# Optimization experiments

Measured on AMD Instinct MI355X. Metric: run time of the kernel, lower is better.

## Reference

```python
import jax, jax.numpy as jnp
import numpy as np
from jax import lax

SLOPE = 0.01  # nn.LeakyReLU default negative slope

def leaky(x):
    return jnp.where(x >= 0, x, SLOPE * x)

def conv2d(x, w, b, pad):
    # x: [N,C,H,W], w: [O,I,kh,kw]
    y = lax.conv_general_dilated(x, w, (1, 1), [(pad, pad), (pad, pad)],
                                 dimension_numbers=('NCHW', 'OIHW', 'NCHW'))
    return y + b[None, :, None, None]

def centered_ifftn(x, axes):
    # np.fft.fftshift(np.fft.ifftn(np.fft.ifftshift(X), norm='ortho'))
    return jnp.fft.fftshift(jnp.fft.ifftn(jnp.fft.ifftshift(x, axes=axes), axes=axes, norm='ortho'), axes=axes)

def setup_inputs() -> dict:
    key = jax.random.key(0)
    ks = jax.random.split(key, 10)
    B, H, W, CK = 8, 640, 368, 32
    return {
        'img':    jax.random.normal(ks[0], (B, 1, H, W), jnp.float32),
        'kspace': jax.random.normal(ks[1], (B, 2, H, W), jnp.float32),
        # k_model1: Conv2d(2, CK, 3, padding=1) + LeakyReLU
        'wk': jax.random.normal(ks[2], (CK, 2, 3, 3), jnp.float32) * 0.1,
        'bk': jnp.zeros((CK,), jnp.float32),
        # conv1: Conv2d(CK, 2, kernel_size=1)
        'w1': jax.random.normal(ks[3], (2, CK, 1, 1), jnp.float32) * 0.1,
        'b1': jnp.zeros((2,), jnp.float32),
        # conv2: Conv2d(2, 1, kernel_size=1)
        'w2': jax.random.normal(ks[4], (1, 2, 1, 1), jnp.float32) * 0.1,
        'b2': jnp.zeros((1,), jnp.float32),
        # i_model1: Conv2d(1, 1, 3, padding=1) + LeakyReLU
        'wi': jax.random.normal(ks[5], (1, 1, 3, 3), jnp.float32) * 0.1,
        'bi': jnp.zeros((1,), jnp.float32),
    }

def reference(img, kspace, wk, bk, w1, b1, w2, b2, wi, bi):
    # k-space branch: k_model1 then conv1 + LeakyReLU
    out1 = leaky(conv2d(leaky(conv2d(kspace, wk, bk, 1)), w1, b1, 0))  # [B,2,H,W]
    # channel 0 = real, channel 1 = imag; ifftn over ALL axes (incl. batch),
    # exactly as the original numpy call with axes=range(out.ndim)
    cplx = out1[:, 0].astype(jnp.complex64) + 1j * out1[:, 1].astype(jnp.complex64)  # [B,H,W]
    im = jnp.abs(centered_ifftn(cplx, (0, 1, 2)))[:, None]  # [B,1,H,W]
    # concat with image, cast to half (torch.cuda.HalfTensor), conv2 + LeakyReLU
    out = jnp.concatenate([im, img], axis=1).astype(jnp.float16)  # [B,2,H,W]
    out = leaky(conv2d(out, w2.astype(jnp.float16), b2.astype(jnp.float16), 0))
    out = out.astype(jnp.float32)  # [B,1,H,W]
    # image-domain model
    return leaky(conv2d(out, wi, bi, 1))  # [B,1,H,W]
```

## Files before the change

### kernel.cpp

```cpp
#include <hip/hip_runtime.h>
#include <hip/hip_fp16.h>
#include <math.h>

#define B_ 8
#define H_ 640
#define W_ 368
#define HW_ (H_*W_)
#define NP_ (B_*H_*W_)

#define FROWS 4
#define HLINES 4
#define HP 645
#define TS 16

typedef __attribute__((ext_vector_type(8))) short v8s;
typedef __attribute__((ext_vector_type(4))) float v4f;

__device__ __forceinline__ float leaky_(float x){ return fmaxf(x, 0.01f*x); }

__device__ __forceinline__ unsigned short f2bf(float x){
    unsigned u = __float_as_uint(x);
    u += 0x7FFFu + ((u >> 16) & 1u);
    return (unsigned short)(u >> 16);
}

__device__ __forceinline__ float2 cadd_(float2 a, float2 b){ return make_float2(a.x+b.x, a.y+b.y); }
__device__ __forceinline__ float2 csub_(float2 a, float2 b){ return make_float2(a.x-b.x, a.y-b.y); }
__device__ __forceinline__ float2 cmul_(float2 a, float c, float s){
    return make_float2(a.x*c - a.y*s, a.x*s + a.y*c);
}
__device__ __forceinline__ float2 cmulv_(float2 a, float2 w){
    return make_float2(a.x*w.x - a.y*w.y, a.x*w.y + a.y*w.x);
}

__device__ __forceinline__ void dft4p_(float2 p0, float2 p1, float2 p2, float2 p3,
                                       float2& z0, float2& z1, float2& z2, float2& z3){
    float2 s0 = cadd_(p0,p2), d0 = csub_(p0,p2);
    float2 s1 = cadd_(p1,p3), d1 = csub_(p1,p3);
    z0 = cadd_(s0,s1);
    z2 = csub_(s0,s1);
    z1 = make_float2(d0.x - d1.y, d0.y + d1.x);
    z3 = make_float2(d0.x + d1.y, d0.y - d1.x);
}

__device__ __forceinline__ void fft16p_(const float2* x, float2* X){
    const float C1 = 0.9238795325112867f, S1 = 0.3826834323650898f;
    const float R  = 0.7071067811865476f;
    float2 Y[4][4];
    #pragma unroll
    for (int b = 0; b < 4; ++b)
        dft4p_(x[b], x[4+b], x[8+b], x[12+b], Y[b][0], Y[b][1], Y[b][2], Y[b][3]);
    Y[1][1] = cmul_(Y[1][1],  C1,  S1);
    Y[1][2] = cmul_(Y[1][2],   R,   R);
    Y[1][3] = cmul_(Y[1][3],  S1,  C1);
    Y[2][1] = cmul_(Y[2][1],   R,   R);
    Y[2][2] = make_float2(-Y[2][2].y, Y[2][2].x);
    Y[2][3] = cmul_(Y[2][3],  -R,   R);
    Y[3][1] = cmul_(Y[3][1],  S1,  C1);
    Y[3][2] = cmul_(Y[3][2],  -R,   R);
    Y[3][3] = cmul_(Y[3][3], -C1, -S1);
    #pragma unroll
    for (int c = 0; c < 4; ++c)
        dft4p_(Y[0][c], Y[1][c], Y[2][c], Y[3][c], X[c], X[c+4], X[c+8], X[c+12]);
}

__device__ __forceinline__ void fft8p_(const float2* x, float2* X){
    const float R = 0.7071067811865476f;
    float2 Y0[4], Y1[4];
    dft4p_(x[0], x[2], x[4], x[6], Y0[0], Y0[1], Y0[2], Y0[3]);
    dft4p_(x[1], x[3], x[5], x[7], Y1[0], Y1[1], Y1[2], Y1[3]);
    float2 T0 = Y1[0];
    float2 T1 = cmul_(Y1[1],  R, R);
    float2 T2 = make_float2(-Y1[2].y, Y1[2].x);
    float2 T3 = cmul_(Y1[3], -R, R);
    X[0] = cadd_(Y0[0], T0);  X[4] = csub_(Y0[0], T0);
    X[1] = cadd_(Y0[1], T1);  X[5] = csub_(Y0[1], T1);
    X[2] = cadd_(Y0[2], T2);  X[6] = csub_(Y0[2], T2);
    X[3] = cadd_(Y0[3], T3);  X[7] = csub_(Y0[3], T3);
}

__global__ void init_tables_kernel(float2* __restrict__ T){
    int i = blockIdx.x*blockDim.x + threadIdx.x;
    if (i >= 1301) return;
    int r, c, modN; int j;
    if      (i <  368){ j = i;        r = j%16; c = j/16; modN = 368; }
    else if (i < 1008){ j = i-368;    r = j%16; c = j/16; modN = 640; }
    else if (i < 1048){ j = i-1008;   r = j%8;  c = j/8;  modN = 40;  }
    else              { j = i-1048;   r = j/11; c = j%11 + 1; modN = 23; }
    int t = (int)(((long long)r * c) % modN);
    if (t > modN/2) t -= modN;
    float ang = (float)(6.283185307179586 * ((double)t / (double)modN));
    float s, co;
    sincosf(ang, &s, &co);
    T[i] = make_float2(co, s);
}

__global__ __launch_bounds__(256) void kfftw_kernel(const float* __restrict__ ksp,
                               const float* __restrict__ wk,
                               const float* __restrict__ bk,
                               const float* __restrict__ w1,
                               const float* __restrict__ b1,
                               const float2* __restrict__ TW368P,
                               const float2* __restrict__ F23P,
                               float2* __restrict__ Bt){
    __shared__ unsigned short Sb[4836];
    __shared__ unsigned short Wr[4*512];
    __shared__ float2 X[FROWS*369];
    int t = threadIdx.x;
    int blk = blockIdx.x;
    int b  = blk / 160;
    int h0 = (blk - b*160) * FROWS;

    for (int seg = 0; seg < 12; ++seg){
        int r = seg >> 1, ic = seg & 1;
        int hh = h0 - 1 + r;
        int ok = ((unsigned)hh < 640u);
        const float* base = ksp + ((size_t)(b*2 + ic)*640 + (ok ? hh : 0))*368;
        for (int col = t; col < 372; col += 256){
            int c = col - 1;
            float v = (ok && (unsigned)c < 368u) ? base[c] : 0.f;
            Sb[seg*372 + col] = f2bf(v);
        }
    }
    for (int i = t; i < 372; i += 256) Sb[4464 + i] = 0;

    int lane = t & 63, wave = t >> 6;
    int oc = lane & 15, q = lane >> 4;
    int l = wave;

    int off[8];
    v8s bf0, bf1, b2f;
    #pragma unroll
    for (int j = 0; j < 8; ++j){
        int kk = q*8 + j;
        if (kk < 18){
            int ic = (kk >= 9) ? 1 : 0;
            int tt = kk - ic*9;
            int ty = tt/3, tx = tt - ty*3;
            off[j] = ((ty + l)*2 + ic)*372 + tx;
            bf0[j] = (short)f2bf(wk[oc*18 + kk]);
            bf1[j] = (short)f2bf(wk[(oc+16)*18 + kk]);
        } else {
            off[j] = 4464;
            bf0[j] = 0; bf1[j] = 0;
        }
        b2f[j] = (oc < 2) ? (short)f2bf(w1[oc*32 + kk]) : (short)0;
    }
    float bk0 = bk[oc], bk1 = bk[oc+16];
    float biasn = (oc == 1) ? b1[1] : b1[0];
    unsigned short* Wrw = Wr + (wave << 9);
    __syncthreads();

    for (int g = 0; g < 23; ++g){
        int w0m = g*16 + oc;
        v8s af;
        #pragma unroll
        for (int j = 0; j < 8; ++j) af[j] = (short)Sb[off[j] + w0m];
        v4f d0 = {0.f,0.f,0.f,0.f}, d1 = {0.f,0.f,0.f,0.f};
        d0 = __builtin_amdgcn_mfma_f32_16x16x32_bf16(af, bf0, d0, 0, 0, 0);
        d1 = __builtin_amdgcn_mfma_f32_16x16x32_bf16(af, bf1, d1, 0, 0, 0);
        #pragma unroll
        for (int r = 0; r < 4; ++r){
            int px = q*4 + r;
            Wrw[px*32 + oc]      = f2bf(leaky_(d0[r] + bk0));
            Wrw[px*32 + 16 + oc] = f2bf(leaky_(d1[r] + bk1));
        }
        asm volatile("s_waitcnt lgkmcnt(0)" ::: "memory");
        const v8s* ap = (const v8s*)(Wrw + oc*32);
        v8s a2 = ap[q];
        v4f d2 = {0.f,0.f,0.f,0.f};
        d2 = __builtin_amdgcn_mfma_f32_16x16x32_bf16(a2, b2f, d2, 0, 0, 0);
        float vals[4], ov[4];
        #pragma unroll
        for (int r = 0; r < 4; ++r){
            vals[r] = leaky_(biasn + d2[r]);
            ov[r] = __shfl_xor(vals[r], 1);
        }
        if (oc == 0){
            int px = g*16 + q*4;
            X[l*369 + px  ] = make_float2( vals[0],  ov[0]);
            X[l*369 + px+1] = make_float2(-vals[1], -ov[1]);
            X[l*369 + px+2] = make_float2( vals[2],  ov[2]);
            X[l*369 + px+3] = make_float2(-vals[3], -ov[3]);
        }
        asm volatile("s_waitcnt lgkmcnt(0)" ::: "memory");
    }
    __syncthreads();

    if (t < 92){
        int ll = t & 3, n2 = t >> 2;
        float2 xr[16], Xo[16];
        #pragma unroll
        for (int n1 = 0; n1 < 16; ++n1) xr[n1] = X[ll*369 + 23*n1 + n2];
        fft16p_(xr, Xo);
        const float2* row = TW368P + n2*16;
        #pragma unroll
        for (int k1 = 0; k1 < 16; ++k1)
            X[ll*369 + 23*k1 + n2] = cmulv_(Xo[k1], row[k1]);
    }
    __syncthreads();

    {
        int ll = t & 3, k1 = (t >> 2) & 15, qr = t >> 6;
        const float2* xp = X + ll*369 + 23*k1;
        float2 x0 = xp[0];
        float2 u[11], d[11];
        #pragma unroll
        for (int m = 1; m <= 11; ++m){
            float2 a = xp[m], bb = xp[23-m];
            u[m-1] = cadd_(a, bb);
            d[m-1] = csub_(a, bb);
        }
        __syncthreads();
        int k2beg = qr*6;
        int k2end = (qr == 3) ? 23 : k2beg + 6;
        for (int k2 = k2beg; k2 < k2end; ++k2){
            const float2* row = F23P + k2*11;
            float re = x0.x, im = x0.y;
            #pragma unroll
            for (int m = 0; m < 11; ++m){
                float c = row[m].x, s = row[m].y;
                re += u[m].x*c - d[m].y*s;
                im += u[m].y*c + d[m].x*s;
            }
            X[ll*369 + k1 + 16*k2] = make_float2(re, im);
        }
    }
    __syncthreads();

    const float sc = 0.052129458158616354f;
    for (int i = t; i < FROWS*368; i += 256){
        int k = i >> 2, ll = i & 3;
        float2 v = X[ll*369 + k];
        float s = (k & 1) ? -sc : sc;
        Bt[((size_t)(b*368 + k))*640 + h0 + ll] = make_float2(v.x*s, v.y*s);
    }
}

__global__ __launch_bounds__(256) void fftH_kernel(const float2* __restrict__ Bt,
                                                   const float2* __restrict__ TW640P,
                                                   const float2* __restrict__ TW40P,
                                                   float2* __restrict__ A2){
    __shared__ float2 X[HLINES*HP];
    int t = threadIdx.x;
    size_t base = (size_t)blockIdx.x * (HLINES*640);

    for (int i = t; i < HLINES*640; i += 256){
        int l = i / 640, n = i - l*640;
        float2 v = Bt[base + i];
        float s = (n & 1) ? -1.f : 1.f;
        X[l*HP + n] = make_float2(v.x*s, v.y*s);
    }
    __syncthreads();

    if (t < 160){
        int l = t & 3, n2 = t >> 2;
        float2 xr[16], Xo[16];
        #pragma unroll
        for (int n1 = 0; n1 < 16; ++n1) xr[n1] = X[l*HP + 40*n1 + n2];
        fft16p_(xr, Xo);
        const float2* row = TW640P + n2*16;
        #pragma unroll
        for (int k1 = 0; k1 < 16; ++k1)
            X[l*HP + 40*k1 + n2] = cmulv_(Xo[k1], row[k1]);
    }
    __syncthreads();

    for (int it = t; it < 320; it += 256){
        int l = it & 3, k1 = (it >> 2) & 15, m2 = it >> 6;
        float2 xr[8], Xo[8];
        #pragma unroll
        for (int m1 = 0; m1 < 8; ++m1) xr[m1] = X[l*HP + 40*k1 + 5*m1 + m2];
        fft8p_(xr, Xo);
        const float2* row = TW40P + m2*8;
        #pragma unroll
        for (int j1 = 0; j1 < 8; ++j1)
            X[l*HP + 40*k1 + 5*j1 + m2] = cmulv_(Xo[j1], row[j1]);
    }
    __syncthreads();

    {
        const float CK1[5] = {1.f,  0.30901699437494745f, -0.8090169943749475f, -0.8090169943749475f,  0.30901699437494745f};
        const float SK1[5] = {0.f,  0.9510565162951535f,   0.5877852522924731f, -0.5877852522924731f, -0.9510565162951535f};
        const float CK2[5] = {1.f, -0.8090169943749475f,   0.30901699437494745f, 0.30901699437494745f, -0.8090169943749475f};
        const float SK2[5] = {0.f,  0.5877852522924731f,  -0.9510565162951535f,  0.9510565162951535f, -0.5877852522924731f};
        int it0 = t, it1 = t + 256;
        int l0 = it0 & 3, k10 = (it0 >> 2) & 15, j10 = it0 >> 6;
        int l1 = it1 & 3, k11 = (it1 >> 2) & 15, j11 = it1 >> 6;
        float2 p0[5], p1[5];
        #pragma unroll
        for (int m2 = 0; m2 < 5; ++m2) p0[m2] = X[l0*HP + 40*k10 + 5*j10 + m2];
        #pragma unroll
        for (int m2 = 0; m2 < 5; ++m2) p1[m2] = X[l1*HP + 40*k11 + 5*j11 + m2];
        __syncthreads();
        float2 u0a = cadd_(p0[1], p0[4]), d0a = csub_(p0[1], p0[4]);
        float2 u0b = cadd_(p0[2], p0[3]), d0b = csub_(p0[2], p0[3]);
        float2 u1a = cadd_(p1[1], p1[4]), d1a = csub_(p1[1], p1[4]);
        float2 u1b = cadd_(p1[2], p1[3]), d1b = csub_(p1[2], p1[3]);
        #pragma unroll
        for (int j2 = 0; j2 < 5; ++j2){
            float c1v = CK1[j2], s1v = SK1[j2], c2v = CK2[j2], s2v = SK2[j2];
            float re0 = p0[0].x + u0a.x*c1v - d0a.y*s1v + u0b.x*c2v - d0b.y*s2v;
            float im0 = p0[0].y + u0a.y*c1v + d0a.x*s1v + u0b.y*c2v + d0b.x*s2v;
            float re1 = p1[0].x + u1a.x*c1v - d1a.y*s1v + u1b.x*c2v - d1b.y*s2v;
            float im1 = p1[0].y + u1a.y*c1v + d1a.x*s1v + u1b.y*c2v + d1b.x*s2v;
            X[l0*HP + k10 + 16*j10 + 128*j2] = make_float2(re0, im0);
            X[l1*HP + k11 + 16*j11 + 128*j2] = make_float2(re1, im1);
        }
    }
    __syncthreads();

    const float sc = 0.03952847075210474f;
    for (int i = t; i < HLINES*640; i += 256){
        int l = i / 640, k = i - l*640;
        float2 v = X[l*HP + k];
        float s = (k & 1) ? -sc : sc;
        A2[base + i] = make_float2(v.x*s, v.y*s);
    }
}

__global__ __launch_bounds__(256) void tail_kernel(const float2* __restrict__ A2,
                                  const float* __restrict__ img,
                                  const float* __restrict__ w2,
                                  const float* __restrict__ b2,
                                  const float* __restrict__ wi,
                                  const float* __restrict__ bi,
                                  float* __restrict__ out){
    __shared__ float Pl[8][TS+2][TS+3];
    int t = threadIdx.x;
    int ty0 = (blockIdx.x / 23) * TS;
    int tx0 = (blockIdx.x % 23) * TS;

    float w2h0 = __half2float(__float2half(w2[0]));
    float w2h1 = __half2float(__float2half(w2[1]));
    float b2h  = __half2float(__float2half(b2[0]));
    const float sc8 = 0.35355339059327373f;

    for (int idx = t; idx < (TS+2)*(TS+2); idx += 256){
        int hx = idx / (TS+2), hy = idx - hx*(TS+2);
        int hh = ty0 - 1 + hy, ww = tx0 - 1 + hx;
        int hc = min(max(hh, 0), H_-1), wc = min(max(ww, 0), W_-1);
        float2 x[8], Xo[8];
        #pragma unroll
        for (int n = 0; n < 8; ++n){
            float2 v = A2[((size_t)(n*368 + wc))*640 + hc];
            float s = (n & 1) ? -1.f : 1.f;
            x[n] = make_float2(v.x*s, v.y*s);
        }
        fft8p_(x, Xo);
        #pragma unroll
        for (int k = 0; k < 8; ++k){
            float s = (k & 1) ? -sc8 : sc8;
            float yr = Xo[k].x * s, yi = Xo[k].y * s;
            float mag = sqrtf(yr*yr + yi*yi);
            Pl[k][hy][hx] = __half2float(__float2half(mag));
        }
    }
    __syncthreads();

    for (int idx = t; idx < (TS+2)*(TS+2); idx += 256){
        int hy = idx / (TS+2), hx = idx - hy*(TS+2);
        int hh = ty0 - 1 + hy, ww = tx0 - 1 + hx;
        bool inb = (hh >= 0) && (hh < H_) && (ww >= 0) && (ww < W_);
        int hc = min(max(hh, 0), H_-1), wc = min(max(ww, 0), W_-1);
        float inbf = inb ? 1.f : 0.f;
        #pragma unroll
        for (int k = 0; k < 8; ++k){
            float g = __half2float(__float2half(img[(size_t)k*HW_ + hc*W_ + wc]));
            float a = Pl[k][hy][hx];
            float o = leaky_(a*w2h0 + g*w2h1 + b2h);
            o = __half2float(__float2half(o));
            Pl[k][hy][hx] = o * inbf;
        }
    }
    __syncthreads();

    int sy = t >> 4, sx = t & 15;
    float wv[9];
    #pragma unroll
    for (int q = 0; q < 9; ++q) wv[q] = wi[q];
    float bi0 = bi[0];
    #pragma unroll
    for (int k = 0; k < 8; ++k){
        float acc = bi0;
        #pragma unroll
        for (int dy = 0; dy < 3; ++dy)
            #pragma unroll
            for (int dx = 0; dx < 3; ++dx)
                acc += wv[dy*3+dx] * Pl[k][sy+dy][sx+dx];
        out[((size_t)k*H_ + ty0+sy)*W_ + tx0+sx] = leaky_(acc);
    }
}

extern "C" void kernel_launch(void* const* d_in, const int* in_sizes, int n_in,
                              void* d_out, int out_size, void* d_ws, size_t ws_size,
                              hipStream_t stream){
    const float* img = (const float*)d_in[0];
    const float* ksp = (const float*)d_in[1];
    const float* wk  = (const float*)d_in[2];
    const float* bk  = (const float*)d_in[3];
    const float* w1  = (const float*)d_in[4];
    const float* b1  = (const float*)d_in[5];
    const float* w2  = (const float*)d_in[6];
    const float* b2  = (const float*)d_in[7];
    const float* wi  = (const float*)d_in[8];
    const float* bi  = (const float*)d_in[9];

    char* ws = (char*)d_ws;
    float2* Bt  = (float2*)(ws + 0);
    float2* A2  = (float2*)(ws + 15073280);
    float2* T   = (float2*)(ws + 30146560);
    float2* TW368P = T + 0;
    float2* TW640P = T + 368;
    float2* TW40P  = T + 1008;
    float2* F23P   = T + 1048;
    float* out  = (float*)d_out;

    init_tables_kernel<<<6, 256, 0, stream>>>(T);

    kfftw_kernel<<<B_*(H_/FROWS), 256, 0, stream>>>(ksp, wk, bk, w1, b1,
                                                    TW368P, F23P, Bt);
    fftH_kernel<<<(B_*W_)/HLINES, 256, 0, stream>>>(Bt, TW640P, TW40P, A2);
    tail_kernel<<<(H_/TS)*(W_/TS), 256, 0, stream>>>(A2, img, w2, b2, wi, bi, out);
}
```

Baseline: 172.4 us.

## Fuse batch-axis FFT and magnitude into H-FFT kernel; widen k-space conv blocks

The H-axis FFT kernel now handles all 8 batch lines for one W column per block and finishes the length-8 batch-axis FFT plus the magnitude in shared memory. It writes a real float magnitude array instead of complex A2, so the tail kernel no longer redoes the batch FFT for every halo pixel and reads half as many bytes. The k-space conv/FFT kernel moves to 512 threads, with two waves splitting each row's column groups and the radix-23 stage spread over more threads. The trade-off is fewer blocks (368) in the H-FFT kernel, more work per block, and higher register pressure.

New measurement: 191.0 us. 1.11x slower.

```diff
diff --git a/kernel.cpp b/kernel.cpp
--- a/kernel.cpp
+++ b/kernel.cpp
@@ -9,7 +9,6 @@
 #define NP_ (B_*H_*W_)
 
 #define FROWS 4
-#define HLINES 4
 #define HP 645
 #define TS 16
 
@@ -95,7 +94,7 @@
     T[i] = make_float2(co, s);
 }
 
-__global__ __launch_bounds__(256) void kfftw_kernel(const float* __restrict__ ksp,
+__global__ __launch_bounds__(512) void kfftw_kernel(const float* __restrict__ ksp,
                                const float* __restrict__ wk,
                                const float* __restrict__ bk,
                                const float* __restrict__ w1,
@@ -104,7 +103,7 @@
                                const float2* __restrict__ F23P,
                                float2* __restrict__ Bt){
     __shared__ unsigned short Sb[4836];
-    __shared__ unsigned short Wr[4*512];
+    __shared__ unsigned short Wr[8*512];
     __shared__ float2 X[FROWS*369];
     int t = threadIdx.x;
     int blk = blockIdx.x;
@@ -116,17 +115,17 @@
         int hh = h0 - 1 + r;
         int ok = ((unsigned)hh < 640u);
         const float* base = ksp + ((size_t)(b*2 + ic)*640 + (ok ? hh : 0))*368;
-        for (int col = t; col < 372; col += 256){
+        for (int col = t; col < 372; col += 512){
             int c = col - 1;
             float v = (ok && (unsigned)c < 368u) ? base[c] : 0.f;
             Sb[seg*372 + col] = f2bf(v);
         }
     }
-    for (int i = t; i < 372; i += 256) Sb[4464 + i] = 0;
+    for (int i = t; i < 372; i += 512) Sb[4464 + i] = 0;
 
     int lane = t & 63, wave = t >> 6;
     int oc = lane & 15, q = lane >> 4;
-    int l = wave;
+    int l = wave >> 1, half = wave & 1;
 
     int off[8];
     v8s bf0, bf1, b2f;
@@ -151,7 +150,9 @@
     unsigned short* Wrw = Wr + (wave << 9);
     __syncthreads();
 
-    for (int g = 0; g < 23; ++g){
+    int gbeg = half ? 12 : 0;
+    int gend = half ? 23 : 12;
+    for (int g = gbeg; g < gend; ++g){
         int w0m = g*16 + oc;
         v8s af;
         #pragma unroll
@@ -201,7 +202,7 @@
     __syncthreads();
 
     {
-        int ll = t & 3, k1 = (t >> 2) & 15, qr = t >> 6;
+        int k1 = t & 15, ll = (t >> 4) & 3, eighth = t >> 6;
         const float2* xp = X + ll*369 + 23*k1;
         float2 x0 = xp[0];
         float2 u[11], d[11];
@@ -212,8 +213,8 @@
             d[m-1] = csub_(a, bb);
         }
         __syncthreads();
-        int k2beg = qr*6;
-        int k2end = (qr == 3) ? 23 : k2beg + 6;
+        int k2beg = eighth*3;
+        int k2end = min(k2beg + 3, 23);
         for (int k2 = k2beg; k2 < k2end; ++k2){
             const float2* row = F23P + k2*11;
             float re = x0.x, im = x0.y;
@@ -229,7 +230,7 @@
     __syncthreads();
 
     const float sc = 0.052129458158616354f;
-    for (int i = t; i < FROWS*368; i += 256){
+    for (int i = t; i < FROWS*368; i += 512){
         int k = i >> 2, ll = i & 3;
         float2 v = X[ll*369 + k];
         float s = (k & 1) ? -sc : sc;
@@ -237,24 +238,24 @@
     }
 }
 
-__global__ __launch_bounds__(256) void fftH_kernel(const float2* __restrict__ Bt,
-                                                   const float2* __restrict__ TW640P,
-                                                   const float2* __restrict__ TW40P,
-                                                   float2* __restrict__ A2){
-    __shared__ float2 X[HLINES*HP];
+__global__ __launch_bounds__(256) void ffthb_kernel(const float2* __restrict__ Bt,
+                                                    const float2* __restrict__ TW640P,
+                                                    const float2* __restrict__ TW40P,
+                                                    float* __restrict__ Mag){
+    __shared__ float2 X[8*HP];
     int t = threadIdx.x;
-    size_t base = (size_t)blockIdx.x * (HLINES*640);
-
-    for (int i = t; i < HLINES*640; i += 256){
+    int w = blockIdx.x;
+
+    for (int i = t; i < 8*640; i += 256){
         int l = i / 640, n = i - l*640;
-        float2 v = Bt[base + i];
+        float2 v = Bt[((size_t)(l*368 + w))*640 + n];
         float s = (n & 1) ? -1.f : 1.f;
         X[l*HP + n] = make_float2(v.x*s, v.y*s);
     }
     __syncthreads();
 
-    if (t < 160){
-        int l = t & 3, n2 = t >> 2;
+    for (int it = t; it < 320; it += 256){
+        int l = it & 7, n2 = it >> 3;
         float2 xr[16], Xo[16];
         #pragma unroll
         for (int n1 = 0; n1 < 16; ++n1) xr[n1] = X[l*HP + 40*n1 + n2];
@@ -266,8 +267,8 @@
     }
     __syncthreads();
 
-    for (int it = t; it < 320; it += 256){
-        int l = it & 3, k1 = (it >> 2) & 15, m2 = it >> 6;
+    for (int it = t; it < 640; it += 256){
+        int l = it & 7, k1 = (it >> 3) & 15, m2 = it >> 7;
         float2 xr[8], Xo[8];
         #pragma unroll
         for (int m1 = 0; m1 < 8; ++m1) xr[m1] = X[l*HP + 40*k1 + 5*m1 + m2];
@@ -284,42 +285,55 @@
         const float SK1[5] = {0.f,  0.9510565162951535f,   0.5877852522924731f, -0.5877852522924731f, -0.9510565162951535f};
         const float CK2[5] = {1.f, -0.8090169943749475f,   0.30901699437494745f, 0.30901699437494745f, -0.8090169943749475f};
         const float SK2[5] = {0.f,  0.5877852522924731f,  -0.9510565162951535f,  0.9510565162951535f, -0.5877852522924731f};
-        int it0 = t, it1 = t + 256;
-        int l0 = it0 & 3, k10 = (it0 >> 2) & 15, j10 = it0 >> 6;
-        int l1 = it1 & 3, k11 = (it1 >> 2) & 15, j11 = it1 >> 6;
-        float2 p0[5], p1[5];
-        #pragma unroll
-        for (int m2 = 0; m2 < 5; ++m2) p0[m2] = X[l0*HP + 40*k10 + 5*j10 + m2];
-        #pragma unroll
-        for (int m2 = 0; m2 < 5; ++m2) p1[m2] = X[l1*HP + 40*k11 + 5*j11 + m2];
+        float2 p[4][5];
+        int ui[4];
+        #pragma unroll
+        for (int i = 0; i < 4; ++i){
+            int u = t + 256*i;
+            ui[u >= 1024 ? 0 : i] = u;
+            ui[i] = u;
+            int l = u & 7, k1 = (u >> 3) & 15, j1 = u >> 7;
+            #pragma unroll
+            for (int m2 = 0; m2 < 5; ++m2)
+                p[i][m2] = X[l*HP + 40*k1 + 5*j1 + m2];
+        }
         __syncthreads();
-        float2 u0a = cadd_(p0[1], p0[4]), d0a = csub_(p0[1], p0[4]);
-        float2 u0b = cadd_(p0[2], p0[3]), d0b = csub_(p0[2], p0[3]);
-        float2 u1a = cadd_(p1[1], p1[4]), d1a = csub_(p1[1], p1[4]);
-        float2 u1b = cadd_(p1[2], p1[3]), d1b = csub_(p1[2], p1[3]);
-        #pragma unroll
-        for (int j2 = 0; j2 < 5; ++j2){
-            float c1v = CK1[j2], s1v = SK1[j2], c2v = CK2[j2], s2v = SK2[j2];
-            float re0 = p0[0].x + u0a.x*c1v - d0a.y*s1v + u0b.x*c2v - d0b.y*s2v;
-            float im0 = p0[0].y + u0a.y*c1v + d0a.x*s1v + u0b.y*c2v + d0b.x*s2v;
-            float re1 = p1[0].x + u1a.x*c1v - d1a.y*s1v + u1b.x*c2v - d1b.y*s2v;
-            float im1 = p1[0].y + u1a.y*c1v + d1a.x*s1v + u1b.y*c2v + d1b.x*s2v;
-            X[l0*HP + k10 + 16*j10 + 128*j2] = make_float2(re0, im0);
-            X[l1*HP + k11 + 16*j11 + 128*j2] = make_float2(re1, im1);
-        }
-    }
-    __syncthreads();
-
-    const float sc = 0.03952847075210474f;
-    for (int i = t; i < HLINES*640; i += 256){
-        int l = i / 640, k = i - l*640;
-        float2 v = X[l*HP + k];
-        float s = (k & 1) ? -sc : sc;
-        A2[base + i] = make_float2(v.x*s, v.y*s);
-    }
-}
-
-__global__ __launch_bounds__(256) void tail_kernel(const float2* __restrict__ A2,
+        #pragma unroll
+        for (int i = 0; i < 4; ++i){
+            int u = ui[i];
+            int l = u & 7, k1 = (u >> 3) & 15, j1 = u >> 7;
+            float2 ua = cadd_(p[i][1], p[i][4]), da = csub_(p[i][1], p[i][4]);
+            float2 ub = cadd_(p[i][2], p[i][3]), db = csub_(p[i][2], p[i][3]);
+            #pragma unroll
+            for (int j2 = 0; j2 < 5; ++j2){
+                float c1v = CK1[j2], s1v = SK1[j2], c2v = CK2[j2], s2v = SK2[j2];
+                float re = p[i][0].x + ua.x*c1v - da.y*s1v + ub.x*c2v - db.y*s2v;
+                float im = p[i][0].y + ua.y*c1v + da.x*s1v + ub.y*c2v + db.x*s2v;
+                X[l*HP + k1 + 16*j1 + 128*j2] = make_float2(re, im);
+            }
+        }
+    }
+    __syncthreads();
+
+    const float SC = 0.013975424859373685f;
+    for (int hh = t; hh < 640; hh += 256){
+        float2 x[8], Xo[8];
+        #pragma unroll
+        for (int l = 0; l < 8; ++l){
+            float2 v = X[l*HP + hh];
+            float s = (l & 1) ? -SC : SC;
+            x[l] = make_float2(v.x*s, v.y*s);
+        }
+        fft8p_(x, Xo);
+        #pragma unroll
+        for (int k = 0; k < 8; ++k){
+            float mag = sqrtf(Xo[k].x*Xo[k].x + Xo[k].y*Xo[k].y);
+            Mag[((size_t)(k*368 + w))*640 + hh] = mag;
+        }
+    }
+}
+
+__global__ __launch_bounds__(256) void tail_kernel(const float* __restrict__ Mag,
                                   const float* __restrict__ img,
                                   const float* __restrict__ w2,
                                   const float* __restrict__ b2,
@@ -334,25 +348,14 @@
     float w2h0 = __half2float(__float2half(w2[0]));
     float w2h1 = __half2float(__float2half(w2[1]));
     float b2h  = __half2float(__float2half(b2[0]));
-    const float sc8 = 0.35355339059327373f;
 
     for (int idx = t; idx < (TS+2)*(TS+2); idx += 256){
         int hx = idx / (TS+2), hy = idx - hx*(TS+2);
         int hh = ty0 - 1 + hy, ww = tx0 - 1 + hx;
         int hc = min(max(hh, 0), H_-1), wc = min(max(ww, 0), W_-1);
-        float2 x[8], Xo[8];
-        #pragma unroll
-        for (int n = 0; n < 8; ++n){
-            float2 v = A2[((size_t)(n*368 + wc))*640 + hc];
-            float s = (n & 1) ? -1.f : 1.f;
-            x[n] = make_float2(v.x*s, v.y*s);
-        }
-        fft8p_(x, Xo);
         #pragma unroll
         for (int k = 0; k < 8; ++k){
-            float s = (k & 1) ? -sc8 : sc8;
-            float yr = Xo[k].x * s, yi = Xo[k].y * s;
-            float mag = sqrtf(yr*yr + yi*yi);
+            float mag = Mag[((size_t)(k*368 + wc))*640 + hc];
             Pl[k][hy][hx] = __half2float(__float2half(mag));
         }
     }
@@ -408,7 +411,7 @@
 
     char* ws = (char*)d_ws;
     float2* Bt  = (float2*)(ws + 0);
-    float2* A2  = (float2*)(ws + 15073280);
+    float*  Mag = (float*)(ws + 15073280);
     float2* T   = (float2*)(ws + 30146560);
     float2* TW368P = T + 0;
     float2* TW640P = T + 368;
@@ -418,8 +421,8 @@
 
     init_tables_kernel<<<6, 256, 0, stream>>>(T);
 
-    kfftw_kernel<<<B_*(H_/FROWS), 256, 0, stream>>>(ksp, wk, bk, w1, b1,
+    kfftw_kernel<<<B_*(H_/FROWS), 512, 0, stream>>>(ksp, wk, bk, w1, b1,
                                                     TW368P, F23P, Bt);
-    fftH_kernel<<<(B_*W_)/HLINES, 256, 0, stream>>>(Bt, TW640P, TW40P, A2);
-    tail_kernel<<<(H_/TS)*(W_/TS), 256, 0, stream>>>(A2, img, w2, b2, wi, bi, out);
-}
+    ffthb_kernel<<<W_, 256, 0, stream>>>(Bt, TW640P, TW40P, Mag);
+    tail_kernel<<<(H_/TS)*(W_/TS), 256, 0, stream>>>(Mag, img, w2, b2, wi, bi, out);
+}
```
